# Kernel optimization log

Hardware: AMD Instinct MI355X
Metric: run time of the kernel (lower is better)

Reference implementation:

```python
import jax, jax.numpy as jnp
import numpy as np

B, T, I, H, F1, C = 65536, 30, 26, 24, 8, 4  # batch, seq_len, input, hidden, fc1, classes


def setup_inputs() -> dict:
    key = jax.random.key(0)
    ks = jax.random.split(key, 9)
    s_ih = 1.0 / np.sqrt(H)
    return {
        "x": jax.random.normal(ks[0], (B, T, I), dtype=jnp.float32),
        "W_ih": jax.random.uniform(ks[1], (3 * H, I), jnp.float32, -s_ih, s_ih),
        "W_hh": jax.random.uniform(ks[2], (3 * H, H), jnp.float32, -s_ih, s_ih),
        "b_ih": jax.random.uniform(ks[3], (3 * H,), jnp.float32, -s_ih, s_ih),
        "b_hh": jax.random.uniform(ks[4], (3 * H,), jnp.float32, -s_ih, s_ih),
        "fc1_w": jax.random.normal(ks[5], (F1, H), jnp.float32) * 0.1,
        "fc1_b": jax.random.normal(ks[6], (F1,), jnp.float32) * 0.1,
        "fc2_w": jax.random.normal(ks[7], (C, F1), jnp.float32) * 0.1,
        "fc2_b": jax.random.normal(ks[8], (C,), jnp.float32) * 0.1,
    }


def reference(x, W_ih, W_hh, b_ih, b_hh, fc1_w, fc1_b, fc2_w, fc2_b):
    # Precompute input projections for all timesteps: (B, T, 3H)
    xp = jnp.einsum("bti,gi->btg", x, W_ih) + b_ih

    def step(h, xt):  # h: (B,H), xt: (B,3H)
        gh = h @ W_hh.T + b_hh  # (B, 3H)
        xr, xz, xn = jnp.split(xt, 3, axis=-1)
        hr, hz, hn = jnp.split(gh, 3, axis=-1)
        r = jax.nn.sigmoid(xr + hr)
        z = jax.nn.sigmoid(xz + hz)
        n = jnp.tanh(xn + r * hn)
        h_new = (1.0 - z) * n + z * h
        return h_new, None

    h0 = jnp.zeros((x.shape[0], W_hh.shape[1]), dtype=x.dtype)
    h, _ = jax.lax.scan(step, h0, jnp.swapaxes(xp, 0, 1))  # final hidden (B, H)

    # eval mode: dropout is identity
    hid = jax.nn.relu(h @ fc1_w.T + fc1_b)
    logits = hid @ fc2_w.T + fc2_b
    return jax.nn.softmax(logits, axis=1)
```

## Files before the change

kernel.cpp:

```cpp
#include <hip/hip_runtime.h>

typedef __bf16 bf16x8 __attribute__((ext_vector_type(8)));
typedef float f32x4 __attribute__((ext_vector_type(4)));

#define T_SEQ 30
#define NIN 26
#define XPITCH 780

#define W_IH 0
#define W_HH 1872
#define B_IH 3600
#define B_HH 3672
#define FC1W 3744
#define FC1B 3936
#define FC2W 3944
#define FC2B 3976

__device__ __forceinline__ float fast_sigmoid(float x) {
    return __builtin_amdgcn_rcpf(1.f + __expf(-x));
}
__device__ __forceinline__ float fast_tanh(float x) {
    return 2.f * __builtin_amdgcn_rcpf(1.f + __expf(-2.f * x)) - 1.f;
}

__global__ __launch_bounds__(256) void gru_kernel(
    const float* __restrict__ x, const float* __restrict__ W_ih,
    const float* __restrict__ W_hh, const float* __restrict__ b_ih,
    const float* __restrict__ b_hh, const float* __restrict__ fc1_w,
    const float* __restrict__ fc1_b, const float* __restrict__ fc2_w,
    const float* __restrict__ fc2_b, float* __restrict__ out)
{
    __shared__ float wbuf[3980];
    __shared__ __attribute__((aligned(16))) __bf16 x_lds[2048];
    __shared__ __attribute__((aligned(16))) __bf16 h_lds[2048];

    const int tid = threadIdx.x;
    const int lane = tid & 63;
    const int w16 = (tid >> 6) << 4;
    const int m = lane & 15;
    const int kg = lane >> 4;
    const int b0 = blockIdx.x << 6;

    for (int i = tid; i < 1872; i += 256) wbuf[W_IH + i] = W_ih[i];
    for (int i = tid; i < 1728; i += 256) wbuf[W_HH + i] = W_hh[i];
    if (tid < 72) wbuf[B_IH + tid] = b_ih[tid];
    else if (tid < 144) wbuf[B_IH + tid] = b_hh[tid - 72];
    if (tid < 192) wbuf[FC1W + tid] = fc1_w[tid];
    if (tid < 8)   wbuf[FC1B + tid] = fc1_b[tid];
    if (tid < 32)  wbuf[FC2W + tid] = fc2_w[tid];
    if (tid < 4)   wbuf[FC2B + tid] = fc2_b[tid];
    for (int i = tid; i < 2048; i += 256) h_lds[i] = (__bf16)0.f;
    __syncthreads();

    bf16x8 bIh[6], bHh[6];
    f32x4 bX[6], bH[6];
    #pragma unroll
    for (int Tn = 0; Tn < 6; ++Tn) {
        const int np = Tn * 16 + m;
        const int gp = np >> 5;
        const int jh = np & 31;
        const bool vc = jh < 24;
        const int g = gp * 24 + jh;
        #pragma unroll
        for (int e = 0; e < 8; ++e) {
            const int k = kg * 8 + e;
            const float vi = (vc && k < 26) ? wbuf[W_IH + g * 26 + k] : 0.f;
            const float vh = (vc && k < 24) ? wbuf[W_HH + g * 24 + k] : 0.f;
            bIh[Tn][e] = (__bf16)vi;
            bHh[Tn][e] = (__bf16)vh;
        }
        const float bx = vc ? wbuf[B_IH + g] : 0.f;
        const float bh = vc ? wbuf[B_HH + g] : 0.f;
        f32x4 vbx = {bx, bx, bx, bx};
        f32x4 vbh = {bh, bh, bh, bh};
        bX[Tn] = vbx;
        bH[Tn] = vbh;
    }

    const int srow = tid >> 2, sch = tid & 3;
    const float* xsrc = x + (size_t)(b0 + srow) * XPITCH + sch * 8;

    {
        float st[8];
        #pragma unroll
        for (int e = 0; e < 8; ++e) {
            const int c = sch * 8 + e;
            st[e] = (c < NIN) ? xsrc[e] : 0.f;
        }
        bf16x8 wv;
        #pragma unroll
        for (int e = 0; e < 8; ++e) wv[e] = (__bf16)st[e];
        *(bf16x8*)&x_lds[sch * 512 + srow * 8] = wv;
    }
    __syncthreads();

    f32x4 hc0 = {0.f, 0.f, 0.f, 0.f}, hc1 = {0.f, 0.f, 0.f, 0.f};
    const int fragoff = kg * 512 + (w16 + m) * 8;
    const int rowbase = w16 + kg * 4;

    #pragma unroll 1
    for (int t = 0; t < T_SEQ; ++t) {
        float nst[8];
        if (t < T_SEQ - 1) {
            const float* p = xsrc + (t + 1) * NIN;
            #pragma unroll
            for (int e = 0; e < 8; ++e) {
                const int c = sch * 8 + e;
                nst[e] = (c < NIN) ? p[e] : 0.f;
            }
        }

        const bf16x8 ax = *(const bf16x8*)&x_lds[fragoff];
        const bf16x8 ah = *(const bf16x8*)&h_lds[fragoff];

        f32x4 aX[6], aH[6];
        #pragma unroll
        for (int Tn = 0; Tn < 6; ++Tn)
            aX[Tn] = __builtin_amdgcn_mfma_f32_16x16x32_bf16(ax, bIh[Tn], bX[Tn], 0, 0, 0);
        #pragma unroll
        for (int Tn = 0; Tn < 6; ++Tn)
            aH[Tn] = __builtin_amdgcn_mfma_f32_16x16x32_bf16(ah, bHh[Tn], bH[Tn], 0, 0, 0);

        #pragma unroll
        for (int tp = 0; tp < 2; ++tp) {
            f32x4& hc = tp ? hc1 : hc0;
            #pragma unroll
            for (int r = 0; r < 4; ++r) {
                const float rg = fast_sigmoid(aX[tp][r] + aH[tp][r]);
                const float zg = fast_sigmoid(aX[2 + tp][r] + aH[2 + tp][r]);
                const float ng = fast_tanh(aX[4 + tp][r] + rg * aH[4 + tp][r]);
                hc[r] = ng + zg * (hc[r] - ng);
            }
        }

        #pragma unroll
        for (int r = 0; r < 4; ++r)
            h_lds[(m >> 3) * 512 + (rowbase + r) * 8 + (m & 7)] = (__bf16)hc0[r];
        if (m < 8) {
            #pragma unroll
            for (int r = 0; r < 4; ++r)
                h_lds[2 * 512 + (rowbase + r) * 8 + m] = (__bf16)hc1[r];
        }

        __syncthreads();
        if (t < T_SEQ - 1) {
            bf16x8 wv;
            #pragma unroll
            for (int e = 0; e < 8; ++e) wv[e] = (__bf16)nst[e];
            *(bf16x8*)&x_lds[sch * 512 + srow * 8] = wv;
        }
        __syncthreads();
    }

    if (lane < 16) {
        const int row = w16 + lane;
        float hv[24];
        #pragma unroll
        for (int j = 0; j < 24; ++j)
            hv[j] = (float)h_lds[(j >> 3) * 512 + row * 8 + (j & 7)];
        float lg[4] = {wbuf[FC2B], wbuf[FC2B + 1], wbuf[FC2B + 2], wbuf[FC2B + 3]};
        #pragma unroll
        for (int o = 0; o < 8; ++o) {
            float s = wbuf[FC1B + o];
            #pragma unroll
            for (int j = 0; j < 24; ++j) s += wbuf[FC1W + o * 24 + j] * hv[j];
            s = fmaxf(s, 0.f);
            #pragma unroll
            for (int c = 0; c < 4; ++c) lg[c] += wbuf[FC2W + c * 8 + o] * s;
        }
        const float mx = fmaxf(fmaxf(lg[0], lg[1]), fmaxf(lg[2], lg[3]));
        const float e0 = __expf(lg[0] - mx), e1 = __expf(lg[1] - mx);
        const float e2 = __expf(lg[2] - mx), e3 = __expf(lg[3] - mx);
        const float inv = __builtin_amdgcn_rcpf(e0 + e1 + e2 + e3);
        f32x4 pr = {e0 * inv, e1 * inv, e2 * inv, e3 * inv};
        *(f32x4*)&out[(size_t)(b0 + row) * 4] = pr;
    }
}

extern "C" void kernel_launch(void* const* d_in, const int* in_sizes, int n_in,
                              void* d_out, int out_size, void* d_ws, size_t ws_size,
                              hipStream_t stream) {
    const float* xx    = (const float*)d_in[0];
    const float* w_ih  = (const float*)d_in[1];
    const float* w_hh  = (const float*)d_in[2];
    const float* bih   = (const float*)d_in[3];
    const float* bhh   = (const float*)d_in[4];
    const float* f1w   = (const float*)d_in[5];
    const float* f1b   = (const float*)d_in[6];
    const float* f2w   = (const float*)d_in[7];
    const float* f2b   = (const float*)d_in[8];
    float* outp = (float*)d_out;

    dim3 grid(65536 / 64), block(256);
    gru_kernel<<<grid, block, 0, stream>>>(xx, w_ih, w_hh, bih, bhh, f1w, f1b, f2w, f2b, outp);
}
```

Baseline: 339.3 us.

## Make GRU recurrence wave-local: direct x fragment loads, per-wave swizzled h buffer, no barriers

Each wave now loads its own x fragment straight from global memory into registers, skipping the shared x staging buffer. It keeps its hidden state in a private, XOR-swizzled LDS slice, which removes both block-wide __syncthreads per timestep. Gate computation is split into two halves so MFMA results feed the nonlinearities sooner, and biases are folded into scalar adds instead of MFMA accumulators. Occupancy is hinted via launch_bounds(256,4). In exchange, global x loads become narrow 8-byte per-lane accesses with less coalescing, and correctness relies on wave-synchronous LDS ordering without explicit barriers.

Measured after the change: 323.0 us. -4.8%, faster.

```diff
diff --git a/kernel.cpp b/kernel.cpp
--- a/kernel.cpp
+++ b/kernel.cpp
@@ -2,6 +2,7 @@
 
 typedef __bf16 bf16x8 __attribute__((ext_vector_type(8)));
 typedef float f32x4 __attribute__((ext_vector_type(4)));
+typedef float f32x2 __attribute__((ext_vector_type(2)));
 
 #define T_SEQ 30
 #define NIN 26
@@ -23,7 +24,7 @@
     return 2.f * __builtin_amdgcn_rcpf(1.f + __expf(-2.f * x)) - 1.f;
 }
 
-__global__ __launch_bounds__(256) void gru_kernel(
+__global__ __launch_bounds__(256, 4) void gru_kernel(
     const float* __restrict__ x, const float* __restrict__ W_ih,
     const float* __restrict__ W_hh, const float* __restrict__ b_ih,
     const float* __restrict__ b_hh, const float* __restrict__ fc1_w,
@@ -31,14 +32,14 @@
     const float* __restrict__ fc2_b, float* __restrict__ out)
 {
     __shared__ float wbuf[3980];
-    __shared__ __attribute__((aligned(16))) __bf16 x_lds[2048];
-    __shared__ __attribute__((aligned(16))) __bf16 h_lds[2048];
+    __shared__ __attribute__((aligned(16))) __bf16 hbuf[4 * 512];
 
     const int tid = threadIdx.x;
     const int lane = tid & 63;
-    const int w16 = (tid >> 6) << 4;
+    const int wid = tid >> 6;
     const int m = lane & 15;
     const int kg = lane >> 4;
+    const int w16 = wid << 4;
     const int b0 = blockIdx.x << 6;
 
     for (int i = tid; i < 1872; i += 256) wbuf[W_IH + i] = W_ih[i];
@@ -49,11 +50,11 @@
     if (tid < 8)   wbuf[FC1B + tid] = fc1_b[tid];
     if (tid < 32)  wbuf[FC2W + tid] = fc2_w[tid];
     if (tid < 4)   wbuf[FC2B + tid] = fc2_b[tid];
-    for (int i = tid; i < 2048; i += 256) h_lds[i] = (__bf16)0.f;
+    for (int i = tid; i < 2048; i += 256) hbuf[i] = (__bf16)0.f;
     __syncthreads();
 
     bf16x8 bIh[6], bHh[6];
-    f32x4 bX[6], bH[6];
+    float bxc[6], bhc[6];
     #pragma unroll
     for (int Tn = 0; Tn < 6; ++Tn) {
         const int np = Tn * 16 + m;
@@ -69,95 +70,105 @@
             bIh[Tn][e] = (__bf16)vi;
             bHh[Tn][e] = (__bf16)vh;
         }
-        const float bx = vc ? wbuf[B_IH + g] : 0.f;
-        const float bh = vc ? wbuf[B_HH + g] : 0.f;
-        f32x4 vbx = {bx, bx, bx, bx};
-        f32x4 vbh = {bh, bh, bh, bh};
-        bX[Tn] = vbx;
-        bH[Tn] = vbh;
-    }
-
-    const int srow = tid >> 2, sch = tid & 3;
-    const float* xsrc = x + (size_t)(b0 + srow) * XPITCH + sch * 8;
-
-    {
-        float st[8];
-        #pragma unroll
-        for (int e = 0; e < 8; ++e) {
-            const int c = sch * 8 + e;
-            st[e] = (c < NIN) ? xsrc[e] : 0.f;
-        }
-        bf16x8 wv;
-        #pragma unroll
-        for (int e = 0; e < 8; ++e) wv[e] = (__bf16)st[e];
-        *(bf16x8*)&x_lds[sch * 512 + srow * 8] = wv;
-    }
-    __syncthreads();
+        bxc[Tn] = vc ? wbuf[B_IH + g] : 0.f;
+        bhc[Tn] = vc ? wbuf[B_HH + g] : 0.f;
+    }
+    const float brz0 = bxc[0] + bhc[0], brz1 = bxc[1] + bhc[1];
+    const float brz2 = bxc[2] + bhc[2], brz3 = bxc[3] + bhc[3];
+
+    __bf16* hw = &hbuf[wid * 512];
+
+    const float* px = x + (size_t)(b0 + w16 + m) * XPITCH + ((kg < 3) ? kg * 8 : 24);
+    const bool full = (kg < 3);
+
+    f32x2 zero2 = {0.f, 0.f};
+    f32x2 xc0, xc1, xc2, xc3;
+    xc1 = zero2; xc2 = zero2; xc3 = zero2;
+    xc0 = *(const f32x2*)px;
+    if (full) {
+        xc1 = *(const f32x2*)(px + 2);
+        xc2 = *(const f32x2*)(px + 4);
+        xc3 = *(const f32x2*)(px + 6);
+    }
 
     f32x4 hc0 = {0.f, 0.f, 0.f, 0.f}, hc1 = {0.f, 0.f, 0.f, 0.f};
-    const int fragoff = kg * 512 + (w16 + m) * 8;
-    const int rowbase = w16 + kg * 4;
-
-    #pragma unroll 1
+    const f32x4 z4 = {0.f, 0.f, 0.f, 0.f};
+
+    const int ra  = m * 32 + ((kg ^ (m >> 2)) << 3);
+    const int wr0 = (kg * 4) * 32 + ((((m >> 3) ^ kg) & 3) << 3) + (m & 7);
+    const int wr1 = (kg * 4) * 32 + (((2 ^ kg) & 3) << 3) + m;
+
+    #pragma unroll 2
     for (int t = 0; t < T_SEQ; ++t) {
-        float nst[8];
+        f32x2 xn0, xn1, xn2, xn3;
+        xn0 = zero2; xn1 = zero2; xn2 = zero2; xn3 = zero2;
         if (t < T_SEQ - 1) {
-            const float* p = xsrc + (t + 1) * NIN;
-            #pragma unroll
-            for (int e = 0; e < 8; ++e) {
-                const int c = sch * 8 + e;
-                nst[e] = (c < NIN) ? p[e] : 0.f;
-            }
-        }
-
-        const bf16x8 ax = *(const bf16x8*)&x_lds[fragoff];
-        const bf16x8 ah = *(const bf16x8*)&h_lds[fragoff];
-
-        f32x4 aX[6], aH[6];
-        #pragma unroll
-        for (int Tn = 0; Tn < 6; ++Tn)
-            aX[Tn] = __builtin_amdgcn_mfma_f32_16x16x32_bf16(ax, bIh[Tn], bX[Tn], 0, 0, 0);
-        #pragma unroll
-        for (int Tn = 0; Tn < 6; ++Tn)
-            aH[Tn] = __builtin_amdgcn_mfma_f32_16x16x32_bf16(ah, bHh[Tn], bH[Tn], 0, 0, 0);
-
-        #pragma unroll
-        for (int tp = 0; tp < 2; ++tp) {
-            f32x4& hc = tp ? hc1 : hc0;
+            const float* p = px + (t + 1) * NIN;
+            xn0 = *(const f32x2*)p;
+            if (full) {
+                xn1 = *(const f32x2*)(p + 2);
+                xn2 = *(const f32x2*)(p + 4);
+                xn3 = *(const f32x2*)(p + 6);
+            }
+        }
+
+        bf16x8 ax;
+        ax[0] = (__bf16)xc0.x; ax[1] = (__bf16)xc0.y;
+        ax[2] = (__bf16)xc1.x; ax[3] = (__bf16)xc1.y;
+        ax[4] = (__bf16)xc2.x; ax[5] = (__bf16)xc2.y;
+        ax[6] = (__bf16)xc3.x; ax[7] = (__bf16)xc3.y;
+
+        const bf16x8 ah = *(const bf16x8*)&hw[ra];
+
+        {
+            f32x4 xr = __builtin_amdgcn_mfma_f32_16x16x32_bf16(ax, bIh[0], z4, 0, 0, 0);
+            f32x4 hr = __builtin_amdgcn_mfma_f32_16x16x32_bf16(ah, bHh[0], z4, 0, 0, 0);
+            f32x4 xz = __builtin_amdgcn_mfma_f32_16x16x32_bf16(ax, bIh[2], z4, 0, 0, 0);
+            f32x4 hz = __builtin_amdgcn_mfma_f32_16x16x32_bf16(ah, bHh[2], z4, 0, 0, 0);
+            f32x4 xn_ = __builtin_amdgcn_mfma_f32_16x16x32_bf16(ax, bIh[4], z4, 0, 0, 0);
+            f32x4 hn = __builtin_amdgcn_mfma_f32_16x16x32_bf16(ah, bHh[4], z4, 0, 0, 0);
             #pragma unroll
             for (int r = 0; r < 4; ++r) {
-                const float rg = fast_sigmoid(aX[tp][r] + aH[tp][r]);
-                const float zg = fast_sigmoid(aX[2 + tp][r] + aH[2 + tp][r]);
-                const float ng = fast_tanh(aX[4 + tp][r] + rg * aH[4 + tp][r]);
-                hc[r] = ng + zg * (hc[r] - ng);
-            }
-        }
-
-        #pragma unroll
-        for (int r = 0; r < 4; ++r)
-            h_lds[(m >> 3) * 512 + (rowbase + r) * 8 + (m & 7)] = (__bf16)hc0[r];
-        if (m < 8) {
+                const float rg = fast_sigmoid(xr[r] + hr[r] + brz0);
+                const float zg = fast_sigmoid(xz[r] + hz[r] + brz2);
+                const float ng = fast_tanh(xn_[r] + bxc[4] + rg * (hn[r] + bhc[4]));
+                hc0[r] = ng + zg * (hc0[r] - ng);
+            }
             #pragma unroll
             for (int r = 0; r < 4; ++r)
-                h_lds[2 * 512 + (rowbase + r) * 8 + m] = (__bf16)hc1[r];
-        }
-
-        __syncthreads();
-        if (t < T_SEQ - 1) {
-            bf16x8 wv;
-            #pragma unroll
-            for (int e = 0; e < 8; ++e) wv[e] = (__bf16)nst[e];
-            *(bf16x8*)&x_lds[sch * 512 + srow * 8] = wv;
-        }
-        __syncthreads();
+                hw[wr0 + r * 32] = (__bf16)hc0[r];
+        }
+
+        {
+            f32x4 xr = __builtin_amdgcn_mfma_f32_16x16x32_bf16(ax, bIh[1], z4, 0, 0, 0);
+            f32x4 hr = __builtin_amdgcn_mfma_f32_16x16x32_bf16(ah, bHh[1], z4, 0, 0, 0);
+            f32x4 xz = __builtin_amdgcn_mfma_f32_16x16x32_bf16(ax, bIh[3], z4, 0, 0, 0);
+            f32x4 hz = __builtin_amdgcn_mfma_f32_16x16x32_bf16(ah, bHh[3], z4, 0, 0, 0);
+            f32x4 xn_ = __builtin_amdgcn_mfma_f32_16x16x32_bf16(ax, bIh[5], z4, 0, 0, 0);
+            f32x4 hn = __builtin_amdgcn_mfma_f32_16x16x32_bf16(ah, bHh[5], z4, 0, 0, 0);
+            #pragma unroll
+            for (int r = 0; r < 4; ++r) {
+                const float rg = fast_sigmoid(xr[r] + hr[r] + brz1);
+                const float zg = fast_sigmoid(xz[r] + hz[r] + brz3);
+                const float ng = fast_tanh(xn_[r] + bxc[5] + rg * (hn[r] + bhc[5]));
+                hc1[r] = ng + zg * (hc1[r] - ng);
+            }
+            if (m < 8) {
+                #pragma unroll
+                for (int r = 0; r < 4; ++r)
+                    hw[wr1 + r * 32] = (__bf16)hc1[r];
+            }
+        }
+
+        xc0 = xn0; xc1 = xn1; xc2 = xn2; xc3 = xn3;
     }
 
     if (lane < 16) {
-        const int row = w16 + lane;
+        const int row = lane;
         float hv[24];
         #pragma unroll
         for (int j = 0; j < 24; ++j)
-            hv[j] = (float)h_lds[(j >> 3) * 512 + row * 8 + (j & 7)];
+            hv[j] = (float)hw[row * 32 + ((((j >> 3) ^ (row >> 2)) & 3) << 3) + (j & 7)];
         float lg[4] = {wbuf[FC2B], wbuf[FC2B + 1], wbuf[FC2B + 2], wbuf[FC2B + 3]};
         #pragma unroll
         for (int o = 0; o < 8; ++o) {
@@ -173,7 +184,7 @@
         const float e2 = __expf(lg[2] - mx), e3 = __expf(lg[3] - mx);
         const float inv = __builtin_amdgcn_rcpf(e0 + e1 + e2 + e3);
         f32x4 pr = {e0 * inv, e1 * inv, e2 * inv, e3 * inv};
-        *(f32x4*)&out[(size_t)(b0 + row) * 4] = pr;
+        *(f32x4*)&out[(size_t)(b0 + w16 + row) * 4] = pr;
     }
 }
 
```
